# Optimization experiments

Hardware: AMD Instinct MI355X
Metric: run time of the kernel (lower is better)

The kernel has to match this reference:

```python
import jax, jax.numpy as jnp
import numpy as np

N = 8192  # input_size
DT = 1.0
TAU1, TAU2, TAU3 = 20.0, 50.0, 100.0


def _corr(a, b):
    # Pearson correlation of two equal-length vectors (torch.corrcoef[0,1]), NaN -> 0
    ac = a - jnp.mean(a)
    bc = b - jnp.mean(b)
    c = jnp.sum(ac * bc) / jnp.sqrt(jnp.sum(ac * ac) * jnp.sum(bc * bc))
    return jnp.where(jnp.isnan(c), jnp.zeros_like(c), c)


def setup_inputs() -> dict:
    key = jax.random.key(0)
    ks = jax.random.split(key, 8)
    return {
        'sensory_motor_input': jax.random.normal(ks[0], (N,), jnp.float32),
        'layer1_state': jax.random.normal(ks[1], (N,), jnp.float32),
        'layer2_state': jax.random.normal(ks[2], (N // 2,), jnp.float32),
        'layer3_state': jax.random.normal(ks[3], (N // 4,), jnp.float32),
        'w12': jax.random.normal(ks[4], (N // 2, N), jnp.float32) * 0.1,
        'w23': jax.random.normal(ks[5], (N // 4, N // 2), jnp.float32) * 0.1,
        'w32': jax.random.normal(ks[6], (N // 2, N // 4), jnp.float32) * 0.1,
        'w21': jax.random.normal(ks[7], (N, N // 2), jnp.float32) * 0.1,
        'correlation_strength': jnp.zeros((), jnp.float32),
        'neural_coherence': jnp.zeros((), jnp.float32),
    }


def reference(sensory_motor_input, layer1_state, layer2_state, layer3_state,
              w12, w23, w32, w21, correlation_strength, neural_coherence):
    # Layer 1: direct sensorimotor, exponential decay toward tanh target
    l1_target = jnp.tanh(sensory_motor_input)
    d1 = 1.0 - DT / TAU1
    l1 = d1 * layer1_state + (1.0 - d1) * l1_target

    # Layer 2: bottom-up + 0.3 * top-down feedback
    l2_in = w12 @ l1 + 0.3 * (w32 @ layer3_state)
    d2 = 1.0 - DT / TAU2
    l2 = d2 * layer2_state + (1.0 - d2) * jnp.tanh(l2_in)

    # Layer 3: meta feedback
    d3 = 1.0 - DT / TAU3
    l3 = d3 * layer3_state + (1.0 - d3) * jnp.tanh(w23 @ l2)

    # Cross-layer correlations (truncate the larger vector)
    c12 = _corr(l1[: l2.shape[0]], l2)
    c23 = _corr(l2[: l3.shape[0]], l3)
    corr_new = 0.9 * correlation_strength + 0.1 * (c12 + c23) / 2.0

    total_activity = jnp.sum(jnp.abs(l1)) + jnp.sum(jnp.abs(l2)) + jnp.sum(jnp.abs(l3))
    activity_variance = jnp.var(jnp.concatenate([l1, l2, l3]), ddof=1)  # torch.var unbiased
    coherence = total_activity / (activity_variance + 1e-6)
    coh_new = 0.9 * neural_coherence + 0.1 * jnp.clip(coherence, 0.0, 10.0)

    hier_activity = total_activity / (N + N // 2 + N // 4)
    return (l1, l2, l3, corr_new, coh_new, hier_activity)
```

## Files before the change

### kernel.cpp

```cpp
#include <hip/hip_runtime.h>
#include <math.h>

#define N1 8192
#define N2 4096
#define N3 2048

typedef float f4 __attribute__((ext_vector_type(4)));

__global__ __launch_bounds__(256) void k_l12(const float* __restrict__ smi,
                                             const float* __restrict__ l1s,
                                             const float* __restrict__ w12,
                                             const float* __restrict__ w32,
                                             const float* __restrict__ l3s,
                                             const float* __restrict__ l2s,
                                             float* __restrict__ l1_out,
                                             float* __restrict__ l2_out) {
    __shared__ float lds_l1[N1];
    __shared__ float ws[4][4];
    const int t = threadIdx.x;
    const int r0 = blockIdx.x * 4;

    const f4* __restrict__ v0 = reinterpret_cast<const f4*>(w32) + (size_t)r0 * (N3 / 4);
    const f4* __restrict__ v1 = v0 + (N3 / 4);
    const f4* __restrict__ v2 = v1 + (N3 / 4);
    const f4* __restrict__ v3 = v2 + (N3 / 4);
    const f4* __restrict__ x3 = reinterpret_cast<const f4*>(l3s);
    float b0 = 0.f, b1 = 0.f, b2 = 0.f, b3 = 0.f;
#pragma unroll
    for (int k = 0; k < (N3 / 4) / 256; ++k) {
        const int i = t + k * 256;
        f4 xv = x3[i];
        f4 u0 = __builtin_nontemporal_load(&v0[i]);
        f4 u1 = __builtin_nontemporal_load(&v1[i]);
        f4 u2 = __builtin_nontemporal_load(&v2[i]);
        f4 u3 = __builtin_nontemporal_load(&v3[i]);
        b0 = fmaf(u0.x, xv.x, fmaf(u0.y, xv.y, fmaf(u0.z, xv.z, fmaf(u0.w, xv.w, b0))));
        b1 = fmaf(u1.x, xv.x, fmaf(u1.y, xv.y, fmaf(u1.z, xv.z, fmaf(u1.w, xv.w, b1))));
        b2 = fmaf(u2.x, xv.x, fmaf(u2.y, xv.y, fmaf(u2.z, xv.z, fmaf(u2.w, xv.w, b2))));
        b3 = fmaf(u3.x, xv.x, fmaf(u3.y, xv.y, fmaf(u3.z, xv.z, fmaf(u3.w, xv.w, b3))));
    }

    {
        const f4* __restrict__ s4 = reinterpret_cast<const f4*>(smi);
        const f4* __restrict__ p4 = reinterpret_cast<const f4*>(l1s);
        f4* __restrict__ d4 = reinterpret_cast<f4*>(lds_l1);
#pragma unroll
        for (int k = 0; k < (N1 / 4) / 256; ++k) {
            const int i = t + k * 256;
            f4 s = s4[i];
            f4 p = p4[i];
            f4 r;
            r.x = fmaf(0.95f, p.x, 0.05f * tanhf(s.x));
            r.y = fmaf(0.95f, p.y, 0.05f * tanhf(s.y));
            r.z = fmaf(0.95f, p.z, 0.05f * tanhf(s.z));
            r.w = fmaf(0.95f, p.w, 0.05f * tanhf(s.w));
            d4[i] = r;
        }
    }
    __syncthreads();

    if (blockIdx.x < 32) {
        const int i = blockIdx.x * 256 + t;
        l1_out[i] = lds_l1[i];
    }

    const f4* __restrict__ w0 = reinterpret_cast<const f4*>(w12) + (size_t)r0 * (N1 / 4);
    const f4* __restrict__ w1 = w0 + (N1 / 4);
    const f4* __restrict__ w2 = w1 + (N1 / 4);
    const f4* __restrict__ w3 = w2 + (N1 / 4);
    const f4* __restrict__ x1 = reinterpret_cast<const f4*>(lds_l1);
    float a0 = 0.f, a1 = 0.f, a2 = 0.f, a3 = 0.f;
#pragma unroll
    for (int k = 0; k < (N1 / 4) / 256; ++k) {
        const int i = t + k * 256;
        f4 xv = x1[i];
        f4 u0 = __builtin_nontemporal_load(&w0[i]);
        f4 u1 = __builtin_nontemporal_load(&w1[i]);
        f4 u2 = __builtin_nontemporal_load(&w2[i]);
        f4 u3 = __builtin_nontemporal_load(&w3[i]);
        a0 = fmaf(u0.x, xv.x, fmaf(u0.y, xv.y, fmaf(u0.z, xv.z, fmaf(u0.w, xv.w, a0))));
        a1 = fmaf(u1.x, xv.x, fmaf(u1.y, xv.y, fmaf(u1.z, xv.z, fmaf(u1.w, xv.w, a1))));
        a2 = fmaf(u2.x, xv.x, fmaf(u2.y, xv.y, fmaf(u2.z, xv.z, fmaf(u2.w, xv.w, a2))));
        a3 = fmaf(u3.x, xv.x, fmaf(u3.y, xv.y, fmaf(u3.z, xv.z, fmaf(u3.w, xv.w, a3))));
    }

    float c0 = fmaf(0.3f, b0, a0);
    float c1 = fmaf(0.3f, b1, a1);
    float c2 = fmaf(0.3f, b2, a2);
    float c3 = fmaf(0.3f, b3, a3);
#pragma unroll
    for (int off = 32; off; off >>= 1) {
        c0 += __shfl_down(c0, off, 64);
        c1 += __shfl_down(c1, off, 64);
        c2 += __shfl_down(c2, off, 64);
        c3 += __shfl_down(c3, off, 64);
    }
    if ((t & 63) == 0) {
        const int w = t >> 6;
        ws[w][0] = c0; ws[w][1] = c1; ws[w][2] = c2; ws[w][3] = c3;
    }
    __syncthreads();
    if (t < 4) {
        const int r = r0 + t;
        float tot = ws[0][t] + ws[1][t] + ws[2][t] + ws[3][t];
        l2_out[r] = 0.98f * l2s[r] + 0.02f * tanhf(tot);
    }
}

__global__ __launch_bounds__(256) void k_l3(const float* __restrict__ w23,
                                            const float* __restrict__ l2,
                                            const float* __restrict__ l3s,
                                            float* __restrict__ l3) {
    __shared__ float ws[4][2];
    const int r0 = blockIdx.x * 2;
    const int t = threadIdx.x;
    const f4* __restrict__ w0 = reinterpret_cast<const f4*>(w23) + (size_t)r0 * (N2 / 4);
    const f4* __restrict__ w1 = w0 + (N2 / 4);
    const f4* __restrict__ x2 = reinterpret_cast<const f4*>(l2);

    float a0 = 0.f, a1 = 0.f;
#pragma unroll
    for (int k = 0; k < (N2 / 4) / 256; ++k) {
        const int i = t + k * 256;
        f4 xv = x2[i];
        f4 u0 = __builtin_nontemporal_load(&w0[i]);
        f4 u1 = __builtin_nontemporal_load(&w1[i]);
        a0 = fmaf(u0.x, xv.x, fmaf(u0.y, xv.y, fmaf(u0.z, xv.z, fmaf(u0.w, xv.w, a0))));
        a1 = fmaf(u1.x, xv.x, fmaf(u1.y, xv.y, fmaf(u1.z, xv.z, fmaf(u1.w, xv.w, a1))));
    }
#pragma unroll
    for (int off = 32; off; off >>= 1) {
        a0 += __shfl_down(a0, off, 64);
        a1 += __shfl_down(a1, off, 64);
    }
    if ((t & 63) == 0) { ws[t >> 6][0] = a0; ws[t >> 6][1] = a1; }
    __syncthreads();
    if (t < 2) {
        const int r = r0 + t;
        float tot = ws[0][t] + ws[1][t] + ws[2][t] + ws[3][t];
        l3[r] = 0.99f * l3s[r] + 0.01f * tanhf(tot);
    }
}

__global__ __launch_bounds__(1024) void k_fin(const float* __restrict__ out,
                                              const float* __restrict__ corr_in,
                                              const float* __restrict__ coh_in,
                                              float* __restrict__ scal) {
    __shared__ double sred[16][13];
    __shared__ double fin[13];
    const int t = threadIdx.x;
    const f4* __restrict__ o4 = reinterpret_cast<const f4*>(out);

    double p[13];
#pragma unroll
    for (int j = 0; j < 13; ++j) p[j] = 0.0;

    for (int i = t; i < 3584; i += 1024) {
        f4 v = o4[i];
#pragma unroll
        for (int c = 0; c < 4; ++c) {
            double d = (double)v[c];
            p[0] += fabs(d); p[1] += d; p[2] += d * d;
        }
    }
    {
        f4 x = o4[t];
        f4 y = o4[2048 + t];
#pragma unroll
        for (int c = 0; c < 4; ++c) {
            double dx = (double)x[c], dy = (double)y[c];
            p[3] += dx; p[4] += dy; p[5] += dx * dx; p[6] += dy * dy; p[7] += dx * dy;
        }
    }
    if (t < 512) {
        f4 x = o4[2048 + t];
        f4 y = o4[3072 + t];
#pragma unroll
        for (int c = 0; c < 4; ++c) {
            double dx = (double)x[c], dy = (double)y[c];
            p[8] += dx; p[9] += dy; p[10] += dx * dx; p[11] += dy * dy; p[12] += dx * dy;
        }
    }

#pragma unroll
    for (int j = 0; j < 13; ++j) {
        double v = p[j];
#pragma unroll
        for (int off = 32; off; off >>= 1) v += __shfl_down(v, off, 64);
        p[j] = v;
    }
    if ((t & 63) == 0) {
        const int w = t >> 6;
#pragma unroll
        for (int j = 0; j < 13; ++j) sred[w][j] = p[j];
    }
    __syncthreads();
    if (t < 13) {
        double s = 0.0;
#pragma unroll
        for (int w = 0; w < 16; ++w) s += sred[w][t];
        fin[t] = s;
    }
    __syncthreads();

    if (t == 0) {
        const double n12 = (double)N2;
        const double n23 = (double)N3;
        const double nall = (double)(N1 + N2 + N3);

        double sxy12 = fin[7] - fin[3] * fin[4] / n12;
        double sxx12 = fin[5] - fin[3] * fin[3] / n12;
        double syy12 = fin[6] - fin[4] * fin[4] / n12;
        double den12 = sqrt(sxx12 * syy12);
        double c12 = (den12 > 0.0 && isfinite(den12)) ? sxy12 / den12 : 0.0;

        double sxy23 = fin[12] - fin[8] * fin[9] / n23;
        double sxx23 = fin[10] - fin[8] * fin[8] / n23;
        double syy23 = fin[11] - fin[9] * fin[9] / n23;
        double den23 = sqrt(sxx23 * syy23);
        double c23 = (den23 > 0.0 && isfinite(den23)) ? sxy23 / den23 : 0.0;

        double corr_new = 0.9 * (double)corr_in[0] + 0.1 * (c12 + c23) * 0.5;

        double total = fin[0];
        double var = (fin[2] - fin[1] * fin[1] / nall) / (nall - 1.0);
        double coh = total / (var + 1e-6);
        coh = fmin(fmax(coh, 0.0), 10.0);
        double coh_new = 0.9 * (double)coh_in[0] + 0.1 * coh;

        scal[0] = (float)corr_new;
        scal[1] = (float)coh_new;
        scal[2] = (float)(total / nall);
    }
}

extern "C" void kernel_launch(void* const* d_in, const int* in_sizes, int n_in,
                              void* d_out, int out_size, void* d_ws, size_t ws_size,
                              hipStream_t stream) {
    const float* smi     = (const float*)d_in[0];
    const float* l1s     = (const float*)d_in[1];
    const float* l2s     = (const float*)d_in[2];
    const float* l3s     = (const float*)d_in[3];
    const float* w12     = (const float*)d_in[4];
    const float* w23     = (const float*)d_in[5];
    const float* w32     = (const float*)d_in[6];
    const float* corr_in = (const float*)d_in[8];
    const float* coh_in  = (const float*)d_in[9];

    float* out = (float*)d_out;
    float* l1 = out;
    float* l2 = out + N1;
    float* l3 = out + N1 + N2;
    float* scal = out + N1 + N2 + N3;

    k_l12<<<dim3(N2 / 4), dim3(256), 0, stream>>>(smi, l1s, w12, w32, l3s, l2s, l1, l2);
    k_l3<<<dim3(N3 / 2), dim3(256), 0, stream>>>(w23, l2, l3s, l3);
    k_fin<<<dim3(1), dim3(1024), 0, stream>>>(out, corr_in, coh_in, scal);
}
```

Measured before the change: 49.05 us.

## Split matvecs into a multi-role first kernel with separate w32 and w23 blocks

The l1 update and w12 matvec, the w32 feedback matvec, and an extra w23 matvec are assigned to different block ranges of one kernel, with partial results written to workspace. A second kernel then combines them into l2, keeps l2 in shared memory and computes the w23·l2 matvec for l3 with 8 rows per block. The extra w23 pass in the first kernel reads w23 against the old layer-2 state, and its result is never consumed, so it looks meant to warm the last-level cache for the second kernel. That extra pass adds a full read of w23. The second kernel runs only 256 blocks and adds a workspace round trip.

```diff
diff --git a/kernel.cpp b/kernel.cpp
--- a/kernel.cpp
+++ b/kernel.cpp
@@ -7,139 +7,212 @@
 
 typedef float f4 __attribute__((ext_vector_type(4)));
 
-__global__ __launch_bounds__(256) void k_l12(const float* __restrict__ smi,
-                                             const float* __restrict__ l1s,
-                                             const float* __restrict__ w12,
-                                             const float* __restrict__ w32,
-                                             const float* __restrict__ l3s,
-                                             const float* __restrict__ l2s,
-                                             float* __restrict__ l1_out,
-                                             float* __restrict__ l2_out) {
-    __shared__ float lds_l1[N1];
-    __shared__ float ws[4][4];
+__device__ __forceinline__ float dot4(f4 u, f4 x, float acc) {
+    return fmaf(u.x, x.x, fmaf(u.y, x.y, fmaf(u.z, x.z, fmaf(u.w, x.w, acc))));
+}
+
+__global__ __launch_bounds__(256) void kA(const float* __restrict__ smi,
+                                          const float* __restrict__ l1s,
+                                          const float* __restrict__ w12,
+                                          const float* __restrict__ w32,
+                                          const float* __restrict__ w23,
+                                          const float* __restrict__ l3s,
+                                          const float* __restrict__ l2s,
+                                          float* __restrict__ a_out,
+                                          float* __restrict__ b_out,
+                                          float* __restrict__ A_out,
+                                          float* __restrict__ l1_out) {
+    __shared__ float lds[N1];
+    const int blk = blockIdx.x;
     const int t = threadIdx.x;
-    const int r0 = blockIdx.x * 4;
-
-    const f4* __restrict__ v0 = reinterpret_cast<const f4*>(w32) + (size_t)r0 * (N3 / 4);
-    const f4* __restrict__ v1 = v0 + (N3 / 4);
-    const f4* __restrict__ v2 = v1 + (N3 / 4);
-    const f4* __restrict__ v3 = v2 + (N3 / 4);
-    const f4* __restrict__ x3 = reinterpret_cast<const f4*>(l3s);
-    float b0 = 0.f, b1 = 0.f, b2 = 0.f, b3 = 0.f;
-#pragma unroll
-    for (int k = 0; k < (N3 / 4) / 256; ++k) {
-        const int i = t + k * 256;
-        f4 xv = x3[i];
-        f4 u0 = __builtin_nontemporal_load(&v0[i]);
-        f4 u1 = __builtin_nontemporal_load(&v1[i]);
-        f4 u2 = __builtin_nontemporal_load(&v2[i]);
-        f4 u3 = __builtin_nontemporal_load(&v3[i]);
-        b0 = fmaf(u0.x, xv.x, fmaf(u0.y, xv.y, fmaf(u0.z, xv.z, fmaf(u0.w, xv.w, b0))));
-        b1 = fmaf(u1.x, xv.x, fmaf(u1.y, xv.y, fmaf(u1.z, xv.z, fmaf(u1.w, xv.w, b1))));
-        b2 = fmaf(u2.x, xv.x, fmaf(u2.y, xv.y, fmaf(u2.z, xv.z, fmaf(u2.w, xv.w, b2))));
-        b3 = fmaf(u3.x, xv.x, fmaf(u3.y, xv.y, fmaf(u3.z, xv.z, fmaf(u3.w, xv.w, b3))));
-    }
+
+    if (blk < 1024) {
+        __shared__ float ws[4][4];
+        const int r0 = blk * 4;
+        {
+            const f4* __restrict__ s4 = reinterpret_cast<const f4*>(smi);
+            const f4* __restrict__ p4 = reinterpret_cast<const f4*>(l1s);
+            f4* __restrict__ d4 = reinterpret_cast<f4*>(lds);
+#pragma unroll
+            for (int k = 0; k < 8; ++k) {
+                const int i = t + k * 256;
+                f4 s = s4[i];
+                f4 p = p4[i];
+                f4 r;
+                r.x = fmaf(0.95f, p.x, 0.05f * tanhf(s.x));
+                r.y = fmaf(0.95f, p.y, 0.05f * tanhf(s.y));
+                r.z = fmaf(0.95f, p.z, 0.05f * tanhf(s.z));
+                r.w = fmaf(0.95f, p.w, 0.05f * tanhf(s.w));
+                d4[i] = r;
+            }
+        }
+        __syncthreads();
+        if (blk < 32) {
+            const int i = blk * 256 + t;
+            l1_out[i] = lds[i];
+        }
+        const f4* __restrict__ w0 = reinterpret_cast<const f4*>(w12) + (size_t)r0 * (N1 / 4);
+        const f4* __restrict__ w1 = w0 + (N1 / 4);
+        const f4* __restrict__ w2 = w1 + (N1 / 4);
+        const f4* __restrict__ w3 = w2 + (N1 / 4);
+        const f4* __restrict__ x1 = reinterpret_cast<const f4*>(lds);
+        float a0 = 0.f, a1 = 0.f, a2 = 0.f, a3 = 0.f;
+#pragma unroll
+        for (int k = 0; k < 8; ++k) {
+            const int i = t + k * 256;
+            f4 xv = x1[i];
+            a0 = dot4(__builtin_nontemporal_load(&w0[i]), xv, a0);
+            a1 = dot4(__builtin_nontemporal_load(&w1[i]), xv, a1);
+            a2 = dot4(__builtin_nontemporal_load(&w2[i]), xv, a2);
+            a3 = dot4(__builtin_nontemporal_load(&w3[i]), xv, a3);
+        }
+#pragma unroll
+        for (int off = 32; off; off >>= 1) {
+            a0 += __shfl_down(a0, off, 64);
+            a1 += __shfl_down(a1, off, 64);
+            a2 += __shfl_down(a2, off, 64);
+            a3 += __shfl_down(a3, off, 64);
+        }
+        if ((t & 63) == 0) {
+            const int w = t >> 6;
+            ws[w][0] = a0; ws[w][1] = a1; ws[w][2] = a2; ws[w][3] = a3;
+        }
+        __syncthreads();
+        if (t < 4) a_out[r0 + t] = ws[0][t] + ws[1][t] + ws[2][t] + ws[3][t];
+    } else if (blk < 1280) {
+        __shared__ float ws[4][16];
+        const int r0 = (blk - 1024) * 16;
+        const f4* __restrict__ base = reinterpret_cast<const f4*>(w32) + (size_t)r0 * (N3 / 4);
+        const f4* __restrict__ x3 = reinterpret_cast<const f4*>(l3s);
+        f4 x0 = x3[t];
+        f4 x1v = x3[t + 256];
+        float acc[16];
+#pragma unroll
+        for (int rr = 0; rr < 16; ++rr) {
+            f4 u0 = __builtin_nontemporal_load(&base[(size_t)rr * (N3 / 4) + t]);
+            f4 u1 = __builtin_nontemporal_load(&base[(size_t)rr * (N3 / 4) + 256 + t]);
+            acc[rr] = dot4(u1, x1v, dot4(u0, x0, 0.f));
+        }
+#pragma unroll
+        for (int rr = 0; rr < 16; ++rr) {
+            float v = acc[rr];
+#pragma unroll
+            for (int off = 32; off; off >>= 1) v += __shfl_down(v, off, 64);
+            acc[rr] = v;
+        }
+        if ((t & 63) == 0) {
+            const int w = t >> 6;
+#pragma unroll
+            for (int rr = 0; rr < 16; ++rr) ws[w][rr] = acc[rr];
+        }
+        __syncthreads();
+        if (t < 16) b_out[r0 + t] = ws[0][t] + ws[1][t] + ws[2][t] + ws[3][t];
+    } else {
+        __shared__ float ws[4][8];
+        const int r0 = (blk - 1280) * 8;
+        const f4* __restrict__ base = reinterpret_cast<const f4*>(w23) + (size_t)r0 * (N2 / 4);
+        const f4* __restrict__ xs = reinterpret_cast<const f4*>(l2s);
+        f4 xv[4];
+#pragma unroll
+        for (int k = 0; k < 4; ++k) xv[k] = xs[t + k * 256];
+        float acc[8];
+#pragma unroll
+        for (int rr = 0; rr < 8; ++rr) {
+            float v = 0.f;
+#pragma unroll
+            for (int k = 0; k < 4; ++k)
+                v = dot4(__builtin_nontemporal_load(&base[(size_t)rr * (N2 / 4) + k * 256 + t]), xv[k], v);
+            acc[rr] = v;
+        }
+#pragma unroll
+        for (int rr = 0; rr < 8; ++rr) {
+            float v = acc[rr];
+#pragma unroll
+            for (int off = 32; off; off >>= 1) v += __shfl_down(v, off, 64);
+            acc[rr] = v;
+        }
+        if ((t & 63) == 0) {
+            const int w = t >> 6;
+#pragma unroll
+            for (int rr = 0; rr < 8; ++rr) ws[w][rr] = acc[rr];
+        }
+        __syncthreads();
+        if (t < 8) A_out[r0 + t] = ws[0][t] + ws[1][t] + ws[2][t] + ws[3][t];
+    }
+}
+
+__global__ __launch_bounds__(256) void kB(const float* __restrict__ w23,
+                                          const float* __restrict__ a_in,
+                                          const float* __restrict__ b_in,
+                                          const float* __restrict__ A_in,
+                                          const float* __restrict__ l2s,
+                                          const float* __restrict__ l3s,
+                                          float* __restrict__ l2_out,
+                                          float* __restrict__ l3_out) {
+    __shared__ float lds_l2[N2];
+    __shared__ float ws[4][8];
+    const int t = threadIdx.x;
+    const int blk = blockIdx.x;
 
     {
-        const f4* __restrict__ s4 = reinterpret_cast<const f4*>(smi);
-        const f4* __restrict__ p4 = reinterpret_cast<const f4*>(l1s);
-        f4* __restrict__ d4 = reinterpret_cast<f4*>(lds_l1);
-#pragma unroll
-        for (int k = 0; k < (N1 / 4) / 256; ++k) {
+        const f4* __restrict__ a4 = reinterpret_cast<const f4*>(a_in);
+        const f4* __restrict__ b4 = reinterpret_cast<const f4*>(b_in);
+        const f4* __restrict__ s4 = reinterpret_cast<const f4*>(l2s);
+        f4* __restrict__ d4 = reinterpret_cast<f4*>(lds_l2);
+#pragma unroll
+        for (int k = 0; k < 4; ++k) {
             const int i = t + k * 256;
-            f4 s = s4[i];
-            f4 p = p4[i];
+            f4 av = a4[i];
+            f4 bv = b4[i];
+            f4 sv = s4[i];
             f4 r;
-            r.x = fmaf(0.95f, p.x, 0.05f * tanhf(s.x));
-            r.y = fmaf(0.95f, p.y, 0.05f * tanhf(s.y));
-            r.z = fmaf(0.95f, p.z, 0.05f * tanhf(s.z));
-            r.w = fmaf(0.95f, p.w, 0.05f * tanhf(s.w));
+            r.x = fmaf(0.98f, sv.x, 0.02f * tanhf(fmaf(0.3f, bv.x, av.x)));
+            r.y = fmaf(0.98f, sv.y, 0.02f * tanhf(fmaf(0.3f, bv.y, av.y)));
+            r.z = fmaf(0.98f, sv.z, 0.02f * tanhf(fmaf(0.3f, bv.z, av.z)));
+            r.w = fmaf(0.98f, sv.w, 0.02f * tanhf(fmaf(0.3f, bv.w, av.w)));
             d4[i] = r;
         }
     }
     __syncthreads();
-
-    if (blockIdx.x < 32) {
-        const int i = blockIdx.x * 256 + t;
-        l1_out[i] = lds_l1[i];
-    }
-
-    const f4* __restrict__ w0 = reinterpret_cast<const f4*>(w12) + (size_t)r0 * (N1 / 4);
-    const f4* __restrict__ w1 = w0 + (N1 / 4);
-    const f4* __restrict__ w2 = w1 + (N1 / 4);
-    const f4* __restrict__ w3 = w2 + (N1 / 4);
-    const f4* __restrict__ x1 = reinterpret_cast<const f4*>(lds_l1);
-    float a0 = 0.f, a1 = 0.f, a2 = 0.f, a3 = 0.f;
-#pragma unroll
-    for (int k = 0; k < (N1 / 4) / 256; ++k) {
-        const int i = t + k * 256;
-        f4 xv = x1[i];
-        f4 u0 = __builtin_nontemporal_load(&w0[i]);
-        f4 u1 = __builtin_nontemporal_load(&w1[i]);
-        f4 u2 = __builtin_nontemporal_load(&w2[i]);
-        f4 u3 = __builtin_nontemporal_load(&w3[i]);
-        a0 = fmaf(u0.x, xv.x, fmaf(u0.y, xv.y, fmaf(u0.z, xv.z, fmaf(u0.w, xv.w, a0))));
-        a1 = fmaf(u1.x, xv.x, fmaf(u1.y, xv.y, fmaf(u1.z, xv.z, fmaf(u1.w, xv.w, a1))));
-        a2 = fmaf(u2.x, xv.x, fmaf(u2.y, xv.y, fmaf(u2.z, xv.z, fmaf(u2.w, xv.w, a2))));
-        a3 = fmaf(u3.x, xv.x, fmaf(u3.y, xv.y, fmaf(u3.z, xv.z, fmaf(u3.w, xv.w, a3))));
-    }
-
-    float c0 = fmaf(0.3f, b0, a0);
-    float c1 = fmaf(0.3f, b1, a1);
-    float c2 = fmaf(0.3f, b2, a2);
-    float c3 = fmaf(0.3f, b3, a3);
-#pragma unroll
-    for (int off = 32; off; off >>= 1) {
-        c0 += __shfl_down(c0, off, 64);
-        c1 += __shfl_down(c1, off, 64);
-        c2 += __shfl_down(c2, off, 64);
-        c3 += __shfl_down(c3, off, 64);
+    if (blk < 16) {
+        const int i = blk * 256 + t;
+        l2_out[i] = lds_l2[i];
+    }
+
+    const int r0 = blk * 8;
+    const f4* __restrict__ base = reinterpret_cast<const f4*>(w23) + (size_t)r0 * (N2 / 4);
+    const f4* __restrict__ xl = reinterpret_cast<const f4*>(lds_l2);
+    f4 xv[4];
+#pragma unroll
+    for (int k = 0; k < 4; ++k) xv[k] = xl[t + k * 256];
+    float acc[8];
+#pragma unroll
+    for (int rr = 0; rr < 8; ++rr) {
+        float v = 0.f;
+#pragma unroll
+        for (int k = 0; k < 4; ++k)
+            v = dot4(base[(size_t)rr * (N2 / 4) + k * 256 + t], xv[k], v);
+        acc[rr] = v;
+    }
+#pragma unroll
+    for (int rr = 0; rr < 8; ++rr) {
+        float v = acc[rr];
+#pragma unroll
+        for (int off = 32; off; off >>= 1) v += __shfl_down(v, off, 64);
+        acc[rr] = v;
     }
     if ((t & 63) == 0) {
         const int w = t >> 6;
-        ws[w][0] = c0; ws[w][1] = c1; ws[w][2] = c2; ws[w][3] = c3;
+#pragma unroll
+        for (int rr = 0; rr < 8; ++rr) ws[w][rr] = acc[rr];
     }
     __syncthreads();
-    if (t < 4) {
+    if (t < 8) {
         const int r = r0 + t;
         float tot = ws[0][t] + ws[1][t] + ws[2][t] + ws[3][t];
-        l2_out[r] = 0.98f * l2s[r] + 0.02f * tanhf(tot);
-    }
-}
-
-__global__ __launch_bounds__(256) void k_l3(const float* __restrict__ w23,
-                                            const float* __restrict__ l2,
-                                            const float* __restrict__ l3s,
-                                            float* __restrict__ l3) {
-    __shared__ float ws[4][2];
-    const int r0 = blockIdx.x * 2;
-    const int t = threadIdx.x;
-    const f4* __restrict__ w0 = reinterpret_cast<const f4*>(w23) + (size_t)r0 * (N2 / 4);
-    const f4* __restrict__ w1 = w0 + (N2 / 4);
-    const f4* __restrict__ x2 = reinterpret_cast<const f4*>(l2);
-
-    float a0 = 0.f, a1 = 0.f;
-#pragma unroll
-    for (int k = 0; k < (N2 / 4) / 256; ++k) {
-        const int i = t + k * 256;
-        f4 xv = x2[i];
-        f4 u0 = __builtin_nontemporal_load(&w0[i]);
-        f4 u1 = __builtin_nontemporal_load(&w1[i]);
-        a0 = fmaf(u0.x, xv.x, fmaf(u0.y, xv.y, fmaf(u0.z, xv.z, fmaf(u0.w, xv.w, a0))));
-        a1 = fmaf(u1.x, xv.x, fmaf(u1.y, xv.y, fmaf(u1.z, xv.z, fmaf(u1.w, xv.w, a1))));
-    }
-#pragma unroll
-    for (int off = 32; off; off >>= 1) {
-        a0 += __shfl_down(a0, off, 64);
-        a1 += __shfl_down(a1, off, 64);
-    }
-    if ((t & 63) == 0) { ws[t >> 6][0] = a0; ws[t >> 6][1] = a1; }
-    __syncthreads();
-    if (t < 2) {
-        const int r = r0 + t;
-        float tot = ws[0][t] + ws[1][t] + ws[2][t] + ws[3][t];
-        l3[r] = 0.99f * l3s[r] + 0.01f * tanhf(tot);
-    }
+        l3_out[r] = 0.99f * l3s[r] + 0.01f * tanhf(tot);
+    }
+    (void)A_in;
 }
 
 __global__ __launch_bounds__(1024) void k_fin(const float* __restrict__ out,
@@ -253,7 +326,12 @@
     float* l3 = out + N1 + N2;
     float* scal = out + N1 + N2 + N3;
 
-    k_l12<<<dim3(N2 / 4), dim3(256), 0, stream>>>(smi, l1s, w12, w32, l3s, l2s, l1, l2);
-    k_l3<<<dim3(N3 / 2), dim3(256), 0, stream>>>(w23, l2, l3s, l3);
+    float* a_ws = (float*)d_ws;
+    float* b_ws = a_ws + N2;
+    float* A_ws = b_ws + N2;
+
+    kA<<<dim3(1536), dim3(256), 0, stream>>>(smi, l1s, w12, w32, w23, l3s, l2s,
+                                             a_ws, b_ws, A_ws, l1);
+    kB<<<dim3(256), dim3(256), 0, stream>>>(w23, a_ws, b_ws, A_ws, l2s, l3s, l2, l3);
     k_fin<<<dim3(1), dim3(1024), 0, stream>>>(out, corr_in, coh_in, scal);
 }
```

Result: slower. 58.72 us (+19.7%).
